# Performance work log

Hardware: AMD Instinct MI355X
Metric: run time of the kernel (lower is better)

Reference implementation:

```python
import jax, jax.numpy as jnp
import numpy as np

BSZ, TSZ, IN_DIM = 32, 1500, 512
G, E = 2, 320            # num_codebooks, num_codebook_entries
OUT_DIM = 768
D = OUT_DIM // G         # entry_dim = 384
TAU = 2.0                # max_temp * decay**0, num_updates starts at 0
EPS = 1e-7
GUMBEL_EPS = 1e-10


def setup_inputs() -> dict:
    key = jax.random.key(0)
    k1, k2, k3, k4 = jax.random.split(key, 4)
    x = jax.random.normal(k1, (BSZ, TSZ, IN_DIM), dtype=jnp.float32)
    W = jax.random.normal(k2, (G * E, IN_DIM), dtype=jnp.float32)  # normal(0,1) init
    b = jnp.zeros((G * E,), dtype=jnp.float32)
    entries = jax.random.uniform(k3, (1, G * E, D), dtype=jnp.float32)
    gumbel_u = jax.random.uniform(k4, (BSZ * TSZ * G, E), dtype=jnp.float32)
    return {"x": x, "W": W, "b": b, "entries": entries, "gumbel_u": gumbel_u}


def reference(x, W, b, entries, gumbel_u):
    bsz, tsz, _ = x.shape
    N = bsz * tsz
    # entry projection -> logits over all codebook entries
    logits = jnp.einsum('btf,ef->bte', x, W) + b            # [B,T,G*E]
    logits = logits.reshape(N * G, E)

    # hard one-hot via argmax (code perplexity stats)
    k = jnp.argmax(logits, axis=-1)                         # [N*G]
    hard_x = jax.nn.one_hot(k, E, dtype=logits.dtype).reshape(N, G, E)
    hard_probs = jnp.mean(hard_x, axis=0)                   # [G,E]
    code_perplexity = jnp.exp(-jnp.sum(hard_probs * jnp.log(hard_probs + EPS), axis=-1)).sum()

    # soft distribution stats (prob perplexity)
    avg_probs = jax.nn.softmax(logits.reshape(N, G, E), axis=-1).mean(axis=0)  # [G,E]
    prob_perplexity = jnp.exp(-jnp.sum(avg_probs * jnp.log(avg_probs + EPS), axis=-1)).sum()

    # gumbel-softmax straight-through (training path)
    g = -jnp.log(-jnp.log(gumbel_u + GUMBEL_EPS) + GUMBEL_EPS)  # gumbel noise from uniforms
    y_soft = jax.nn.softmax((logits + g) / TAU, axis=-1)        # [N*G,E]
    k_g = jnp.argmax(y_soft, axis=-1)
    y_hard = jax.nn.one_hot(k_g, E, dtype=y_soft.dtype)
    y = y_hard + y_soft - jax.lax.stop_gradient(y_soft)        # straight-through

    cb = y.reshape(N, G * E)
    # one-hot-weighted sum over codebook entries
    quantized = jnp.einsum('nge,ged->ngd', y.reshape(N, G, E), entries.reshape(G, E, D))
    quantized = quantized.reshape(bsz, tsz, G * D)             # [B,T,OUT_DIM]
    return quantized, cb, code_perplexity, prob_perplexity
```

## Files before the change

kernel.cpp:

```cpp
#include <hip/hip_runtime.h>
#include <math.h>
#include <stdint.h>

#define NROWS 48000
#define KDIM 512
#define NE 320
#define GE 640
#define DDIM 384
#define ODIM 768
#define CB_OFF 36864000ul
#define SC_OFF 67584000ul
#define MARGIN 4e-3f

using f16x8 = __attribute__((ext_vector_type(8))) _Float16;
using f32x4 = __attribute__((ext_vector_type(4))) float;

#define GLD16(gp, lp)                                                          \
    __builtin_amdgcn_global_load_lds(                                          \
        (const __attribute__((address_space(1))) uint32_t*)(gp),               \
        (__attribute__((address_space(3))) uint32_t*)(lp), 16, 0, 0)

__global__ __launch_bounds__(256) void split16(const float* __restrict__ src,
                                               _Float16* __restrict__ hi,
                                               _Float16* __restrict__ lo,
                                               int n8)
{
    int i = blockIdx.x * 256 + threadIdx.x;
    if (i >= n8) return;
    float4 v0 = *((const float4*)src + 2 * (size_t)i);
    float4 v1 = *((const float4*)src + 2 * (size_t)i + 1);
    float x[8] = {v0.x, v0.y, v0.z, v0.w, v1.x, v1.y, v1.z, v1.w};
    f16x8 h, l;
    #pragma unroll
    for (int k = 0; k < 8; ++k) {
        _Float16 hh = (_Float16)x[k];
        h[k] = hh;
        l[k] = (_Float16)(x[k] - (float)hh);
    }
    *(f16x8*)(hi + (size_t)i * 8) = h;
    *(f16x8*)(lo + (size_t)i * 8) = l;
}

__global__ __launch_bounds__(256) void gemm_cvt(
    const float* __restrict__ X,
    const _Float16* __restrict__ Wh, const _Float16* __restrict__ Wl,
    const float* __restrict__ bvec, float* __restrict__ Lout)
{
    __shared__ _Float16 lds[16384];
    _Float16* Ahs = lds;
    _Float16* Als = lds + 4096;
    _Float16* Bhs = lds + 8192;
    _Float16* Bls = lds + 12288;

    const int bid = blockIdx.x;
    const int q8 = 1875 / 8, r8 = 1875 % 8;
    const int xcd = bid & 7, wi = bid >> 3;
    const int wg = (xcd < r8 ? xcd * (q8 + 1) : r8 * (q8 + 1) + (xcd - r8) * q8) + wi;
    const int bm = wg / 5, bn = wg % 5;

    const int tid = threadIdx.x;
    const int wid = tid >> 6, lane = tid & 63;
    const int fr = lane & 15, fq = lane >> 4;
    const int wm = (wid >> 1) * 64, wn = (wid & 1) * 64;

    const float*     Ag  = X  + (size_t)(bm * 128) * KDIM;
    const _Float16*  Bhg = Wh + (size_t)(bn * 128) * KDIM;
    const _Float16*  Blg = Wl + (size_t)(bn * 128) * KDIM;

    f32x4 acc[4][4];
    #pragma unroll
    for (int i = 0; i < 4; ++i)
        #pragma unroll
        for (int j = 0; j < 4; ++j)
            acc[i][j] = (f32x4){0.f, 0.f, 0.f, 0.f};

    for (int kk = 0; kk < 16; ++kk) {
        const int kh = kk * 32;
        #pragma unroll
        for (int q = 0; q < 2; ++q) {
            const int c = wid * 2 + q;
            const int srow = lane >> 2, sc8 = (lane & 3) * 8;
            const size_t go = (size_t)(c * 16 + srow) * KDIM + kh + sc8;
            GLD16(Bhg + go, Bhs + c * 512);
            GLD16(Blg + go, Bls + c * 512);
        }
        #pragma unroll
        for (int c = 0; c < 2; ++c) {
            const int idx8 = c * 256 + tid;
            const int row = idx8 >> 2, k8 = (idx8 & 3) * 8;
            const float4* xp = (const float4*)(Ag + (size_t)row * KDIM + kh + k8);
            float4 v0 = xp[0], v1 = xp[1];
            float xs[8] = {v0.x, v0.y, v0.z, v0.w, v1.x, v1.y, v1.z, v1.w};
            f16x8 h, l;
            #pragma unroll
            for (int q = 0; q < 8; ++q) {
                _Float16 hh = (_Float16)xs[q];
                h[q] = hh;
                l[q] = (_Float16)(xs[q] - (float)hh);
            }
            *(f16x8*)&Ahs[row * 32 + k8] = h;
            *(f16x8*)&Als[row * 32 + k8] = l;
        }
        __syncthreads();

        f16x8 ah[4], al[4], bh[4], bl[4];
        #pragma unroll
        for (int i = 0; i < 4; ++i) {
            const int ro = (wm + i * 16 + fr) * 32 + fq * 8;
            ah[i] = *(const f16x8*)&Ahs[ro];
            al[i] = *(const f16x8*)&Als[ro];
            const int co = (wn + i * 16 + fr) * 32 + fq * 8;
            bh[i] = *(const f16x8*)&Bhs[co];
            bl[i] = *(const f16x8*)&Bls[co];
        }
        #pragma unroll
        for (int i = 0; i < 4; ++i)
            #pragma unroll
            for (int j = 0; j < 4; ++j) {
                acc[i][j] = __builtin_amdgcn_mfma_f32_16x16x32_f16(ah[i], bh[j], acc[i][j], 0, 0, 0);
                acc[i][j] = __builtin_amdgcn_mfma_f32_16x16x32_f16(ah[i], bl[j], acc[i][j], 0, 0, 0);
                acc[i][j] = __builtin_amdgcn_mfma_f32_16x16x32_f16(al[i], bh[j], acc[i][j], 0, 0, 0);
            }
        __syncthreads();
    }

    #pragma unroll
    for (int i = 0; i < 4; ++i) {
        #pragma unroll
        for (int r = 0; r < 4; ++r) {
            const int m = bm * 128 + wm + i * 16 + fq * 4 + r;
            float* orow = Lout + (size_t)m * GE + bn * 128 + wn;
            #pragma unroll
            for (int j = 0; j < 4; ++j) {
                const int n = bn * 128 + wn + j * 16 + fr;
                orow[j * 16 + fr] = acc[i][j][r] + bvec[n];
            }
        }
    }
}

__device__ __forceinline__ bool better(float a, int ia, float b, int ib) {
    return (a > b) || (a == b && ia < ib);
}

__device__ __forceinline__ void top2_half(const float* v, int il,
                                          float& v1, int& i1, float& v2, int& i2)
{
    v1 = -3.4e38f; i1 = 0x7fffffff;
    v2 = -3.4e38f; i2 = 0x7fffffff;
    #pragma unroll
    for (int i = 0; i < 10; ++i) {
        int e = il + 32 * i;
        float x = v[i];
        if (better(x, e, v1, i1)) { v2 = v1; i2 = i1; v1 = x; i1 = e; }
        else if (better(x, e, v2, i2)) { v2 = x; i2 = e; }
    }
    #pragma unroll
    for (int m = 1; m <= 16; m <<= 1) {
        float ov1 = __shfl_xor(v1, m); int oi1 = __shfl_xor(i1, m);
        float ov2 = __shfl_xor(v2, m); int oi2 = __shfl_xor(i2, m);
        float lv; int li;
        if (better(ov1, oi1, v1, i1)) { lv = v1; li = i1; v1 = ov1; i1 = oi1; }
        else { lv = ov1; li = oi1; }
        if (better(lv, li, v2, i2)) { v2 = lv; i2 = li; }
        if (better(ov2, oi2, v2, i2)) { v2 = ov2; i2 = oi2; }
    }
}

__device__ int resolve2(const float* __restrict__ X, const float* __restrict__ W,
                        const float* __restrict__ bvec, const float* __restrict__ Urow,
                        int n, int h, int c1, int c2, bool gum, int il)
{
    const float* xr = X + (size_t)n * KDIM;
    const float* w1 = W + (size_t)(h * NE + c1) * KDIM;
    const float* w2 = W + (size_t)(h * NE + c2) * KDIM;
    double d1 = 0.0, d2 = 0.0;
    #pragma unroll
    for (int j = 0; j < 16; ++j) {
        int k = il + 32 * j;
        double xv = (double)xr[k];
        d1 += xv * (double)w1[k];
        d2 += xv * (double)w2[k];
    }
    #pragma unroll
    for (int m = 1; m <= 16; m <<= 1) {
        d1 += __shfl_xor(d1, m);
        d2 += __shfl_xor(d2, m);
    }
    d1 += (double)bvec[h * NE + c1];
    d2 += (double)bvec[h * NE + c2];
    if (gum) {
        d1 += -log(-log((double)Urow[c1] + 1e-10) + 1e-10);
        d2 += -log(-log((double)Urow[c2] + 1e-10) + 1e-10);
    }
    return (d2 > d1 || (d2 == d1 && c2 < c1)) ? c2 : c1;
}

__global__ __launch_bounds__(256) void epilogue_kernel(
    const float* __restrict__ X, const float* __restrict__ W,
    const float* __restrict__ bvec, const float* __restrict__ entries,
    const float* __restrict__ gumbel, float* __restrict__ out,
    float* __restrict__ gavgp, unsigned int* __restrict__ gcnt)
{
    __shared__ float s_avgp[GE];
    __shared__ unsigned int s_cnt[GE];
    const int tid = threadIdx.x;
    for (int i = tid; i < GE; i += 256) { s_avgp[i] = 0.f; s_cnt[i] = 0u; }
    __syncthreads();

    const int wave = tid >> 6, lane = tid & 63;
    const int h = lane >> 5, il = lane & 31;

    float accp[10];
    #pragma unroll
    for (int i = 0; i < 10; ++i) accp[i] = 0.f;

    float* cb = out + CB_OFF;

    for (int rr = 0; rr < 8; ++rr) {
        const int n = blockIdx.x * 32 + wave * 8 + rr;
        float* Lrow = cb + (size_t)n * GE + h * NE;
        const float* Urow = gumbel + (size_t)(2 * n + h) * NE;

        float lg[10], zg[10];
        #pragma unroll
        for (int i = 0; i < 10; ++i) {
            int e = il + 32 * i;
            lg[i] = Lrow[e];
            float gn = -logf(-logf(Urow[e] + 1e-10f) + 1e-10f);
            zg[i] = lg[i] + gn;
        }

        float pv1, pv2; int pi1, pi2;
        top2_half(lg, il, pv1, pi1, pv2, pi2);
        float gv1, gv2; int gi1, gi2;
        top2_half(zg, il, gv1, gi1, gv2, gi2);

        int k_plain = pi1;
        if (pv1 - pv2 < MARGIN)
            k_plain = resolve2(X, W, bvec, Urow, n, h, pi1, pi2, false, il);
        int k_g = gi1;
        if (gv1 - gv2 < MARGIN)
            k_g = resolve2(X, W, bvec, Urow, n, h, gi1, gi2, true, il);

        float s = 0.f, ex[10];
        #pragma unroll
        for (int i = 0; i < 10; ++i) { ex[i] = expf(lg[i] - pv1); s += ex[i]; }
        #pragma unroll
        for (int m = 1; m <= 16; m <<= 1) s += __shfl_xor(s, m);
        float inv = 1.f / s;
        #pragma unroll
        for (int i = 0; i < 10; ++i) accp[i] += ex[i] * inv;

        if (il == 0) atomicAdd(&s_cnt[h * NE + k_plain], 1u);

        #pragma unroll
        for (int i = 0; i < 10; ++i) {
            int e = il + 32 * i;
            Lrow[e] = (e == k_g) ? 1.f : 0.f;
        }
        const float* ent = entries + (size_t)(h * NE + k_g) * DDIM;
        float* qrow = out + (size_t)n * ODIM + h * DDIM;
        #pragma unroll
        for (int j = 0; j < 12; ++j) {
            int d = il + 32 * j;
            qrow[d] = ent[d];
        }
    }

    #pragma unroll
    for (int i = 0; i < 10; ++i)
        atomicAdd(&s_avgp[h * NE + il + 32 * i], accp[i]);
    __syncthreads();
    for (int i = tid; i < GE; i += 256) {
        atomicAdd(&gavgp[i], s_avgp[i]);
        unsigned int c = s_cnt[i];
        if (c) atomicAdd(&gcnt[i], c);
    }
}

__global__ void finalize_kernel(const float* __restrict__ gavgp,
                                const unsigned int* __restrict__ gcnt,
                                float* __restrict__ out)
{
    __shared__ double sc[GE], sp[GE];
    const int t = threadIdx.x;
    if (t < GE) {
        double hp = (double)gcnt[t] * (1.0 / 48000.0);
        sc[t] = hp * log(hp + 1e-7);
        double ap = (double)gavgp[t] * (1.0 / 48000.0);
        sp[t] = ap * log(ap + 1e-7);
    }
    __syncthreads();
    if (t == 0) {
        double c0 = 0, c1 = 0, p0 = 0, p1 = 0;
        for (int e = 0; e < NE; ++e) { c0 += sc[e]; p0 += sp[e]; }
        for (int e = NE; e < GE; ++e) { c1 += sc[e]; p1 += sp[e]; }
        out[SC_OFF]     = (float)(exp(-c0) + exp(-c1));
        out[SC_OFF + 1] = (float)(exp(-p0) + exp(-p1));
    }
}

extern "C" void kernel_launch(void* const* d_in, const int* in_sizes, int n_in,
                              void* d_out, int out_size, void* d_ws, size_t ws_size,
                              hipStream_t stream)
{
    const float* X       = (const float*)d_in[0];
    const float* Wf      = (const float*)d_in[1];
    const float* bvec    = (const float*)d_in[2];
    const float* entries = (const float*)d_in[3];
    const float* gumbel  = (const float*)d_in[4];
    float* out = (float*)d_out;

    float* gavgp = (float*)d_ws;
    unsigned int* gcnt = (unsigned int*)((char*)d_ws + 2560);
    _Float16* Wh = (_Float16*)((char*)d_ws + 8192);
    _Float16* Wl = (_Float16*)((char*)d_ws + 8192 + 655360);

    hipMemsetAsync(d_ws, 0, 8192, stream);
    split16<<<160, 256, 0, stream>>>(Wf, Wh, Wl, 40960);
    gemm_cvt<<<1875, 256, 0, stream>>>(X, Wh, Wl, bvec, out + CB_OFF);
    epilogue_kernel<<<1500, 256, 0, stream>>>(X, Wf, bvec, entries, gumbel, out, gavgp, gcnt);
    finalize_kernel<<<1, 640, 0, stream>>>(gavgp, gcnt, out);
}
```

Before: 274.7 us.

## Fuse epilogue into GEMM via per-panel completion counters

```diff
diff --git a/kernel.cpp b/kernel.cpp
--- a/kernel.cpp
+++ b/kernel.cpp
@@ -41,10 +41,70 @@
     *(f16x8*)(lo + (size_t)i * 8) = l;
 }
 
-__global__ __launch_bounds__(256) void gemm_cvt(
-    const float* __restrict__ X,
+__device__ __forceinline__ bool better(float a, int ia, float b, int ib) {
+    return (a > b) || (a == b && ia < ib);
+}
+
+__device__ __forceinline__ void top2_half(const float* v, int il,
+                                          float& v1, int& i1, float& v2, int& i2)
+{
+    v1 = -3.4e38f; i1 = 0x7fffffff;
+    v2 = -3.4e38f; i2 = 0x7fffffff;
+    #pragma unroll
+    for (int i = 0; i < 10; ++i) {
+        int e = il + 32 * i;
+        float x = v[i];
+        if (better(x, e, v1, i1)) { v2 = v1; i2 = i1; v1 = x; i1 = e; }
+        else if (better(x, e, v2, i2)) { v2 = x; i2 = e; }
+    }
+    #pragma unroll
+    for (int m = 1; m <= 16; m <<= 1) {
+        float ov1 = __shfl_xor(v1, m); int oi1 = __shfl_xor(i1, m);
+        float ov2 = __shfl_xor(v2, m); int oi2 = __shfl_xor(i2, m);
+        float lv; int li;
+        if (better(ov1, oi1, v1, i1)) { lv = v1; li = i1; v1 = ov1; i1 = oi1; }
+        else { lv = ov1; li = oi1; }
+        if (better(lv, li, v2, i2)) { v2 = lv; i2 = li; }
+        if (better(ov2, oi2, v2, i2)) { v2 = ov2; i2 = oi2; }
+    }
+}
+
+__device__ int resolve2(const float* __restrict__ X, const float* __restrict__ W,
+                        const float* __restrict__ bvec, const float* __restrict__ Urow,
+                        int n, int h, int c1, int c2, bool gum, int il)
+{
+    const float* xr = X + (size_t)n * KDIM;
+    const float* w1 = W + (size_t)(h * NE + c1) * KDIM;
+    const float* w2 = W + (size_t)(h * NE + c2) * KDIM;
+    double d1 = 0.0, d2 = 0.0;
+    #pragma unroll
+    for (int j = 0; j < 16; ++j) {
+        int k = il + 32 * j;
+        double xv = (double)xr[k];
+        d1 += xv * (double)w1[k];
+        d2 += xv * (double)w2[k];
+    }
+    #pragma unroll
+    for (int m = 1; m <= 16; m <<= 1) {
+        d1 += __shfl_xor(d1, m);
+        d2 += __shfl_xor(d2, m);
+    }
+    d1 += (double)bvec[h * NE + c1];
+    d2 += (double)bvec[h * NE + c2];
+    if (gum) {
+        d1 += -log(-log((double)Urow[c1] + 1e-10) + 1e-10);
+        d2 += -log(-log((double)Urow[c2] + 1e-10) + 1e-10);
+    }
+    return (d2 > d1 || (d2 == d1 && c2 < c1)) ? c2 : c1;
+}
+
+__global__ __launch_bounds__(256) void gemm_fused(
+    const float* __restrict__ X, const float* __restrict__ Wf,
     const _Float16* __restrict__ Wh, const _Float16* __restrict__ Wl,
-    const float* __restrict__ bvec, float* __restrict__ Lout)
+    const float* __restrict__ bvec, const float* __restrict__ entries,
+    const float* __restrict__ gumbel, float* __restrict__ out,
+    float* __restrict__ gavgp, unsigned int* __restrict__ gcnt,
+    unsigned int* __restrict__ panelcnt)
 {
     __shared__ _Float16 lds[16384];
     _Float16* Ahs = lds;
@@ -124,158 +184,106 @@
         __syncthreads();
     }
 
+    float* cb = out + CB_OFF;
     #pragma unroll
     for (int i = 0; i < 4; ++i) {
         #pragma unroll
         for (int r = 0; r < 4; ++r) {
             const int m = bm * 128 + wm + i * 16 + fq * 4 + r;
-            float* orow = Lout + (size_t)m * GE + bn * 128 + wn;
+            float* orow = cb + (size_t)m * GE + bn * 128 + wn;
             #pragma unroll
-            for (int j = 0; j < 4; ++j) {
-                const int n = bn * 128 + wn + j * 16 + fr;
-                orow[j * 16 + fr] = acc[i][j][r] + bvec[n];
+            for (int j = 0; j < 4; ++j)
+                orow[j * 16 + fr] = acc[i][j][r] + bvec[bn * 128 + wn + j * 16 + fr];
+        }
+    }
+
+    __syncthreads();
+    float*    s_avgp = (float*)lds;
+    unsigned* s_cnt  = (unsigned*)((char*)lds + 2560);
+    unsigned* s_own  = (unsigned*)((char*)lds + 5120);
+    for (int i = tid; i < GE; i += 256) { s_avgp[i] = 0.f; s_cnt[i] = 0u; }
+    if (tid < 4) {
+        __threadfence();
+        unsigned old = __hip_atomic_fetch_add(&panelcnt[bm * 4 + tid], 1u,
+                                              __ATOMIC_ACQ_REL,
+                                              __HIP_MEMORY_SCOPE_AGENT);
+        unsigned o = (old == 4u) ? 1u : 0u;
+        if (o) __threadfence();
+        s_own[tid] = o;
+    }
+    __syncthreads();
+
+    const bool anyown = (s_own[0] | s_own[1] | s_own[2] | s_own[3]) != 0u;
+    if (anyown) {
+        const int h2 = lane >> 5, il = lane & 31;
+        float accp[10];
+        #pragma unroll
+        for (int i = 0; i < 10; ++i) accp[i] = 0.f;
+
+        for (int sp = 0; sp < 4; ++sp) {
+            if (!s_own[sp]) continue;
+            for (int rr = 0; rr < 8; ++rr) {
+                const int n = bm * 128 + sp * 32 + wid * 8 + rr;
+                float* Lrow = cb + (size_t)n * GE + h2 * NE;
+                const float* Urow = gumbel + (size_t)(2 * n + h2) * NE;
+
+                float lg[10], zg[10];
+                #pragma unroll
+                for (int i = 0; i < 10; ++i) {
+                    int e = il + 32 * i;
+                    lg[i] = Lrow[e];
+                    float gn = -logf(-logf(Urow[e] + 1e-10f) + 1e-10f);
+                    zg[i] = lg[i] + gn;
+                }
+
+                float pv1, pv2; int pi1, pi2;
+                top2_half(lg, il, pv1, pi1, pv2, pi2);
+                float gv1, gv2; int gi1, gi2;
+                top2_half(zg, il, gv1, gi1, gv2, gi2);
+
+                int k_plain = pi1;
+                if (pv1 - pv2 < MARGIN)
+                    k_plain = resolve2(X, Wf, bvec, Urow, n, h2, pi1, pi2, false, il);
+                int k_g = gi1;
+                if (gv1 - gv2 < MARGIN)
+                    k_g = resolve2(X, Wf, bvec, Urow, n, h2, gi1, gi2, true, il);
+
+                float s = 0.f, ex[10];
+                #pragma unroll
+                for (int i = 0; i < 10; ++i) { ex[i] = expf(lg[i] - pv1); s += ex[i]; }
+                #pragma unroll
+                for (int m = 1; m <= 16; m <<= 1) s += __shfl_xor(s, m);
+                float inv = 1.f / s;
+                #pragma unroll
+                for (int i = 0; i < 10; ++i) accp[i] += ex[i] * inv;
+
+                if (il == 0) atomicAdd(&s_cnt[h2 * NE + k_plain], 1u);
+
+                #pragma unroll
+                for (int i = 0; i < 10; ++i) {
+                    int e = il + 32 * i;
+                    Lrow[e] = (e == k_g) ? 1.f : 0.f;
+                }
+                const float* ent = entries + (size_t)(h2 * NE + k_g) * DDIM;
+                float* qrow = out + (size_t)n * ODIM + h2 * DDIM;
+                #pragma unroll
+                for (int j = 0; j < 12; ++j) {
+                    int d = il + 32 * j;
+                    qrow[d] = ent[d];
+                }
             }
         }
-    }
-}
-
-__device__ __forceinline__ bool better(float a, int ia, float b, int ib) {
-    return (a > b) || (a == b && ia < ib);
-}
-
-__device__ __forceinline__ void top2_half(const float* v, int il,
-                                          float& v1, int& i1, float& v2, int& i2)
-{
-    v1 = -3.4e38f; i1 = 0x7fffffff;
-    v2 = -3.4e38f; i2 = 0x7fffffff;
-    #pragma unroll
-    for (int i = 0; i < 10; ++i) {
-        int e = il + 32 * i;
-        float x = v[i];
-        if (better(x, e, v1, i1)) { v2 = v1; i2 = i1; v1 = x; i1 = e; }
-        else if (better(x, e, v2, i2)) { v2 = x; i2 = e; }
-    }
-    #pragma unroll
-    for (int m = 1; m <= 16; m <<= 1) {
-        float ov1 = __shfl_xor(v1, m); int oi1 = __shfl_xor(i1, m);
-        float ov2 = __shfl_xor(v2, m); int oi2 = __shfl_xor(i2, m);
-        float lv; int li;
-        if (better(ov1, oi1, v1, i1)) { lv = v1; li = i1; v1 = ov1; i1 = oi1; }
-        else { lv = ov1; li = oi1; }
-        if (better(lv, li, v2, i2)) { v2 = lv; i2 = li; }
-        if (better(ov2, oi2, v2, i2)) { v2 = ov2; i2 = oi2; }
-    }
-}
-
-__device__ int resolve2(const float* __restrict__ X, const float* __restrict__ W,
-                        const float* __restrict__ bvec, const float* __restrict__ Urow,
-                        int n, int h, int c1, int c2, bool gum, int il)
-{
-    const float* xr = X + (size_t)n * KDIM;
-    const float* w1 = W + (size_t)(h * NE + c1) * KDIM;
-    const float* w2 = W + (size_t)(h * NE + c2) * KDIM;
-    double d1 = 0.0, d2 = 0.0;
-    #pragma unroll
-    for (int j = 0; j < 16; ++j) {
-        int k = il + 32 * j;
-        double xv = (double)xr[k];
-        d1 += xv * (double)w1[k];
-        d2 += xv * (double)w2[k];
-    }
-    #pragma unroll
-    for (int m = 1; m <= 16; m <<= 1) {
-        d1 += __shfl_xor(d1, m);
-        d2 += __shfl_xor(d2, m);
-    }
-    d1 += (double)bvec[h * NE + c1];
-    d2 += (double)bvec[h * NE + c2];
-    if (gum) {
-        d1 += -log(-log((double)Urow[c1] + 1e-10) + 1e-10);
-        d2 += -log(-log((double)Urow[c2] + 1e-10) + 1e-10);
-    }
-    return (d2 > d1 || (d2 == d1 && c2 < c1)) ? c2 : c1;
-}
-
-__global__ __launch_bounds__(256) void epilogue_kernel(
-    const float* __restrict__ X, const float* __restrict__ W,
-    const float* __restrict__ bvec, const float* __restrict__ entries,
-    const float* __restrict__ gumbel, float* __restrict__ out,
-    float* __restrict__ gavgp, unsigned int* __restrict__ gcnt)
-{
-    __shared__ float s_avgp[GE];
-    __shared__ unsigned int s_cnt[GE];
-    const int tid = threadIdx.x;
-    for (int i = tid; i < GE; i += 256) { s_avgp[i] = 0.f; s_cnt[i] = 0u; }
-    __syncthreads();
-
-    const int wave = tid >> 6, lane = tid & 63;
-    const int h = lane >> 5, il = lane & 31;
-
-    float accp[10];
-    #pragma unroll
-    for (int i = 0; i < 10; ++i) accp[i] = 0.f;
-
-    float* cb = out + CB_OFF;
-
-    for (int rr = 0; rr < 8; ++rr) {
-        const int n = blockIdx.x * 32 + wave * 8 + rr;
-        float* Lrow = cb + (size_t)n * GE + h * NE;
-        const float* Urow = gumbel + (size_t)(2 * n + h) * NE;
-
-        float lg[10], zg[10];
-        #pragma unroll
-        for (int i = 0; i < 10; ++i) {
-            int e = il + 32 * i;
-            lg[i] = Lrow[e];
-            float gn = -logf(-logf(Urow[e] + 1e-10f) + 1e-10f);
-            zg[i] = lg[i] + gn;
-        }
-
-        float pv1, pv2; int pi1, pi2;
-        top2_half(lg, il, pv1, pi1, pv2, pi2);
-        float gv1, gv2; int gi1, gi2;
-        top2_half(zg, il, gv1, gi1, gv2, gi2);
-
-        int k_plain = pi1;
-        if (pv1 - pv2 < MARGIN)
-            k_plain = resolve2(X, W, bvec, Urow, n, h, pi1, pi2, false, il);
-        int k_g = gi1;
-        if (gv1 - gv2 < MARGIN)
-            k_g = resolve2(X, W, bvec, Urow, n, h, gi1, gi2, true, il);
-
-        float s = 0.f, ex[10];
-        #pragma unroll
-        for (int i = 0; i < 10; ++i) { ex[i] = expf(lg[i] - pv1); s += ex[i]; }
-        #pragma unroll
-        for (int m = 1; m <= 16; m <<= 1) s += __shfl_xor(s, m);
-        float inv = 1.f / s;
-        #pragma unroll
-        for (int i = 0; i < 10; ++i) accp[i] += ex[i] * inv;
-
-        if (il == 0) atomicAdd(&s_cnt[h * NE + k_plain], 1u);
-
-        #pragma unroll
-        for (int i = 0; i < 10; ++i) {
-            int e = il + 32 * i;
-            Lrow[e] = (e == k_g) ? 1.f : 0.f;
-        }
-        const float* ent = entries + (size_t)(h * NE + k_g) * DDIM;
-        float* qrow = out + (size_t)n * ODIM + h * DDIM;
-        #pragma unroll
-        for (int j = 0; j < 12; ++j) {
-            int d = il + 32 * j;
-            qrow[d] = ent[d];
-        }
-    }
-
-    #pragma unroll
-    for (int i = 0; i < 10; ++i)
-        atomicAdd(&s_avgp[h * NE + il + 32 * i], accp[i]);
-    __syncthreads();
-    for (int i = tid; i < GE; i += 256) {
-        atomicAdd(&gavgp[i], s_avgp[i]);
-        unsigned int c = s_cnt[i];
-        if (c) atomicAdd(&gcnt[i], c);
+
+        #pragma unroll
+        for (int i = 0; i < 10; ++i)
+            atomicAdd(&s_avgp[h2 * NE + il + 32 * i], accp[i]);
+        __syncthreads();
+        for (int i = tid; i < GE; i += 256) {
+            float a = s_avgp[i];
+            if (a != 0.f) atomicAdd(&gavgp[i], a);
+            unsigned c = s_cnt[i];
+            if (c) atomicAdd(&gcnt[i], c);
+        }
     }
 }
 
@@ -314,12 +322,13 @@
 
     float* gavgp = (float*)d_ws;
     unsigned int* gcnt = (unsigned int*)((char*)d_ws + 2560);
-    _Float16* Wh = (_Float16*)((char*)d_ws + 8192);
-    _Float16* Wl = (_Float16*)((char*)d_ws + 8192 + 655360);
-
-    hipMemsetAsync(d_ws, 0, 8192, stream);
+    unsigned int* panelcnt = (unsigned int*)((char*)d_ws + 5120);
+    _Float16* Wh = (_Float16*)((char*)d_ws + 11264);
+    _Float16* Wl = (_Float16*)((char*)d_ws + 11264 + 655360);
+
+    hipMemsetAsync(d_ws, 0, 11264, stream);
     split16<<<160, 256, 0, stream>>>(Wf, Wh, Wl, 40960);
-    gemm_cvt<<<1875, 256, 0, stream>>>(X, Wh, Wl, bvec, out + CB_OFF);
-    epilogue_kernel<<<1500, 256, 0, stream>>>(X, Wf, bvec, entries, gumbel, out, gavgp, gcnt);
+    gemm_fused<<<1875, 256, 0, stream>>>(X, Wf, Wh, Wl, bvec, entries,
+                                         gumbel, out, gavgp, gcnt, panelcnt);
     finalize_kernel<<<1, 640, 0, stream>>>(gavgp, gcnt, out);
 }
```

After: 690.5 us. 2.51x slower.

## Vectorize epilogue with float4 loads/stores and 16-lane row groups

Applied to the files above, without the earlier changes.

```diff
diff --git a/kernel.cpp b/kernel.cpp
--- a/kernel.cpp
+++ b/kernel.cpp
@@ -143,52 +143,51 @@
     return (a > b) || (a == b && ia < ib);
 }
 
-__device__ __forceinline__ void top2_half(const float* v, int il,
-                                          float& v1, int& i1, float& v2, int& i2)
-{
-    v1 = -3.4e38f; i1 = 0x7fffffff;
-    v2 = -3.4e38f; i2 = 0x7fffffff;
-    #pragma unroll
-    for (int i = 0; i < 10; ++i) {
-        int e = il + 32 * i;
-        float x = v[i];
-        if (better(x, e, v1, i1)) { v2 = v1; i2 = i1; v1 = x; i1 = e; }
-        else if (better(x, e, v2, i2)) { v2 = x; i2 = e; }
-    }
-    #pragma unroll
-    for (int m = 1; m <= 16; m <<= 1) {
+__device__ __forceinline__ void t2merge(float& v1, int& i1, float& v2, int& i2,
+                                        float ov1, int oi1, float ov2, int oi2)
+{
+    if (better(ov1, oi1, v1, i1)) {
+        float tv = v1; int ti = i1;
+        v1 = ov1; i1 = oi1;
+        if (better(ov2, oi2, tv, ti)) { v2 = ov2; i2 = oi2; }
+        else                          { v2 = tv;  i2 = ti;  }
+    } else if (better(ov1, oi1, v2, i2)) {
+        v2 = ov1; i2 = oi1;
+    }
+}
+
+__device__ __forceinline__ void bfly16(float& v1, int& i1, float& v2, int& i2)
+{
+    #pragma unroll
+    for (int m = 1; m <= 8; m <<= 1) {
         float ov1 = __shfl_xor(v1, m); int oi1 = __shfl_xor(i1, m);
         float ov2 = __shfl_xor(v2, m); int oi2 = __shfl_xor(i2, m);
-        float lv; int li;
-        if (better(ov1, oi1, v1, i1)) { lv = v1; li = i1; v1 = ov1; i1 = oi1; }
-        else { lv = ov1; li = oi1; }
-        if (better(lv, li, v2, i2)) { v2 = lv; i2 = li; }
-        if (better(ov2, oi2, v2, i2)) { v2 = ov2; i2 = oi2; }
-    }
-}
-
-__device__ int resolve2(const float* __restrict__ X, const float* __restrict__ W,
-                        const float* __restrict__ bvec, const float* __restrict__ Urow,
-                        int n, int h, int c1, int c2, bool gum, int il)
+        t2merge(v1, i1, v2, i2, ov1, oi1, ov2, oi2);
+    }
+}
+
+__device__ int resolve16(const float* __restrict__ X, const float* __restrict__ W,
+                         const float* __restrict__ bvec, const float* __restrict__ Urow,
+                         int n, int cb, int c1, int c2, bool gum, int l)
 {
     const float* xr = X + (size_t)n * KDIM;
-    const float* w1 = W + (size_t)(h * NE + c1) * KDIM;
-    const float* w2 = W + (size_t)(h * NE + c2) * KDIM;
+    const float* w1 = W + (size_t)(cb * NE + c1) * KDIM;
+    const float* w2 = W + (size_t)(cb * NE + c2) * KDIM;
     double d1 = 0.0, d2 = 0.0;
     #pragma unroll
-    for (int j = 0; j < 16; ++j) {
-        int k = il + 32 * j;
+    for (int j = 0; j < 32; ++j) {
+        int k = l + 16 * j;
         double xv = (double)xr[k];
         d1 += xv * (double)w1[k];
         d2 += xv * (double)w2[k];
     }
     #pragma unroll
-    for (int m = 1; m <= 16; m <<= 1) {
+    for (int m = 1; m <= 8; m <<= 1) {
         d1 += __shfl_xor(d1, m);
         d2 += __shfl_xor(d2, m);
     }
-    d1 += (double)bvec[h * NE + c1];
-    d2 += (double)bvec[h * NE + c2];
+    d1 += (double)bvec[cb * NE + c1];
+    d2 += (double)bvec[cb * NE + c2];
     if (gum) {
         d1 += -log(-log((double)Urow[c1] + 1e-10) + 1e-10);
         d2 += -log(-log((double)Urow[c2] + 1e-10) + 1e-10);
@@ -208,69 +207,82 @@
     for (int i = tid; i < GE; i += 256) { s_avgp[i] = 0.f; s_cnt[i] = 0u; }
     __syncthreads();
 
-    const int wave = tid >> 6, lane = tid & 63;
-    const int h = lane >> 5, il = lane & 31;
-
-    float accp[10];
-    #pragma unroll
-    for (int i = 0; i < 10; ++i) accp[i] = 0.f;
-
-    float* cb = out + CB_OFF;
+    const int wid = tid >> 6, lane = tid & 63;
+    const int qw = lane >> 4, l = lane & 15;
+    const int cb = qw & 1, rsub = qw >> 1;
+
+    float accp[20];
+    #pragma unroll
+    for (int t = 0; t < 20; ++t) accp[t] = 0.f;
 
     for (int rr = 0; rr < 8; ++rr) {
-        const int n = blockIdx.x * 32 + wave * 8 + rr;
-        float* Lrow = cb + (size_t)n * GE + h * NE;
-        const float* Urow = gumbel + (size_t)(2 * n + h) * NE;
-
-        float lg[10], zg[10];
-        #pragma unroll
-        for (int i = 0; i < 10; ++i) {
-            int e = il + 32 * i;
-            lg[i] = Lrow[e];
-            float gn = -logf(-logf(Urow[e] + 1e-10f) + 1e-10f);
-            zg[i] = lg[i] + gn;
-        }
-
-        float pv1, pv2; int pi1, pi2;
-        top2_half(lg, il, pv1, pi1, pv2, pi2);
-        float gv1, gv2; int gi1, gi2;
-        top2_half(zg, il, gv1, gi1, gv2, gi2);
-
-        int k_plain = pi1;
-        if (pv1 - pv2 < MARGIN)
-            k_plain = resolve2(X, W, bvec, Urow, n, h, pi1, pi2, false, il);
+        const int n = blockIdx.x * 64 + wid * 16 + rr * 2 + rsub;
+        float* Lrow = out + CB_OFF + (size_t)n * GE + cb * NE;
+        const float* Urow = gumbel + (size_t)(2 * n + cb) * NE;
+
+        float lg[20];
+        float v1 = -3.4e38f, v2 = -3.4e38f; int i1 = 0x7fffffff, i2 = 0x7fffffff;
+        float g1 = -3.4e38f, g2 = -3.4e38f; int gi1 = 0x7fffffff, gi2 = 0x7fffffff;
+        #pragma unroll
+        for (int q = 0; q < 5; ++q) {
+            float4 lv = *(const float4*)(Lrow + l * 4 + q * 64);
+            float4 uv = *(const float4*)(Urow + l * 4 + q * 64);
+            float lx[4] = {lv.x, lv.y, lv.z, lv.w};
+            float ux[4] = {uv.x, uv.y, uv.z, uv.w};
+            #pragma unroll
+            for (int c = 0; c < 4; ++c) {
+                float x = lx[c];
+                lg[q * 4 + c] = x;
+                int e = l * 4 + q * 64 + c;
+                if (better(x, e, v1, i1)) { v2 = v1; i2 = i1; v1 = x; i1 = e; }
+                else if (better(x, e, v2, i2)) { v2 = x; i2 = e; }
+                float z = x + (-logf(-logf(ux[c] + 1e-10f) + 1e-10f));
+                if (better(z, e, g1, gi1)) { g2 = g1; gi2 = gi1; g1 = z; gi1 = e; }
+                else if (better(z, e, g2, gi2)) { g2 = z; gi2 = e; }
+            }
+        }
+        bfly16(v1, i1, v2, i2);
+        bfly16(g1, gi1, g2, gi2);
+
+        int k_plain = i1;
+        if (v1 - v2 < MARGIN)
+            k_plain = resolve16(X, W, bvec, Urow, n, cb, i1, i2, false, l);
         int k_g = gi1;
-        if (gv1 - gv2 < MARGIN)
-            k_g = resolve2(X, W, bvec, Urow, n, h, gi1, gi2, true, il);
-
-        float s = 0.f, ex[10];
-        #pragma unroll
-        for (int i = 0; i < 10; ++i) { ex[i] = expf(lg[i] - pv1); s += ex[i]; }
-        #pragma unroll
-        for (int m = 1; m <= 16; m <<= 1) s += __shfl_xor(s, m);
+        if (g1 - g2 < MARGIN)
+            k_g = resolve16(X, W, bvec, Urow, n, cb, gi1, gi2, true, l);
+
+        float s = 0.f, ex[20];
+        #pragma unroll
+        for (int t = 0; t < 20; ++t) { ex[t] = expf(lg[t] - v1); s += ex[t]; }
+        #pragma unroll
+        for (int m = 1; m <= 8; m <<= 1) s += __shfl_xor(s, m);
         float inv = 1.f / s;
         #pragma unroll
-        for (int i = 0; i < 10; ++i) accp[i] += ex[i] * inv;
-
-        if (il == 0) atomicAdd(&s_cnt[h * NE + k_plain], 1u);
-
-        #pragma unroll
-        for (int i = 0; i < 10; ++i) {
-            int e = il + 32 * i;
-            Lrow[e] = (e == k_g) ? 1.f : 0.f;
-        }
-        const float* ent = entries + (size_t)(h * NE + k_g) * DDIM;
-        float* qrow = out + (size_t)n * ODIM + h * DDIM;
-        #pragma unroll
-        for (int j = 0; j < 12; ++j) {
-            int d = il + 32 * j;
-            qrow[d] = ent[d];
-        }
-    }
-
-    #pragma unroll
-    for (int i = 0; i < 10; ++i)
-        atomicAdd(&s_avgp[h * NE + il + 32 * i], accp[i]);
+        for (int t = 0; t < 20; ++t) accp[t] += ex[t] * inv;
+
+        if (l == 0) atomicAdd(&s_cnt[cb * NE + k_plain], 1u);
+
+        #pragma unroll
+        for (int q = 0; q < 5; ++q) {
+            const int c0 = l * 4 + q * 64;
+            float4 v;
+            v.x = (c0     == k_g) ? 1.f : 0.f;
+            v.y = (c0 + 1 == k_g) ? 1.f : 0.f;
+            v.z = (c0 + 2 == k_g) ? 1.f : 0.f;
+            v.w = (c0 + 3 == k_g) ? 1.f : 0.f;
+            *(float4*)(Lrow + c0) = v;
+        }
+        const float4* ent = (const float4*)(entries + (size_t)(cb * NE + k_g) * DDIM);
+        float4* qrow = (float4*)(out + (size_t)n * ODIM + cb * DDIM);
+        #pragma unroll
+        for (int t = 0; t < 6; ++t) qrow[l + t * 16] = ent[l + t * 16];
+    }
+
+    #pragma unroll
+    for (int q = 0; q < 5; ++q)
+        #pragma unroll
+        for (int c = 0; c < 4; ++c)
+            atomicAdd(&s_avgp[cb * NE + l * 4 + q * 64 + c], accp[q * 4 + c]);
     __syncthreads();
     for (int i = tid; i < GE; i += 256) {
         atomicAdd(&gavgp[i], s_avgp[i]);
@@ -320,6 +332,6 @@
     hipMemsetAsync(d_ws, 0, 8192, stream);
     split16<<<160, 256, 0, stream>>>(Wf, Wh, Wl, 40960);
     gemm_cvt<<<1875, 256, 0, stream>>>(X, Wh, Wl, bvec, out + CB_OFF);
-    epilogue_kernel<<<1500, 256, 0, stream>>>(X, Wf, bvec, entries, gumbel, out, gavgp, gcnt);
+    epilogue_kernel<<<750, 256, 0, stream>>>(X, Wf, bvec, entries, gumbel, out, gavgp, gcnt);
     finalize_kernel<<<1, 640, 0, stream>>>(gavgp, gcnt, out);
 }
```

Result: slower. 316.1 us (+15.0%).

## Drop low-part of X in split-fp16 GEMM, widen fp64 top-3 argmax fallback

Applied to the files above, without the earlier changes.

```diff
diff --git a/kernel.cpp b/kernel.cpp
--- a/kernel.cpp
+++ b/kernel.cpp
@@ -10,7 +10,7 @@
 #define ODIM 768
 #define CB_OFF 36864000ul
 #define SC_OFF 67584000ul
-#define MARGIN 4e-3f
+#define MARGIN 0.04f
 
 using f16x8 = __attribute__((ext_vector_type(8))) _Float16;
 using f32x4 = __attribute__((ext_vector_type(4))) float;
@@ -46,11 +46,10 @@
     const _Float16* __restrict__ Wh, const _Float16* __restrict__ Wl,
     const float* __restrict__ bvec, float* __restrict__ Lout)
 {
-    __shared__ _Float16 lds[16384];
+    __shared__ _Float16 lds[12288];
     _Float16* Ahs = lds;
-    _Float16* Als = lds + 4096;
-    _Float16* Bhs = lds + 8192;
-    _Float16* Bls = lds + 12288;
+    _Float16* Bhs = lds + 4096;
+    _Float16* Bls = lds + 8192;
 
     const int bid = blockIdx.x;
     const int q8 = 1875 / 8, r8 = 1875 % 8;
@@ -91,24 +90,18 @@
             const float4* xp = (const float4*)(Ag + (size_t)row * KDIM + kh + k8);
             float4 v0 = xp[0], v1 = xp[1];
             float xs[8] = {v0.x, v0.y, v0.z, v0.w, v1.x, v1.y, v1.z, v1.w};
-            f16x8 h, l;
+            f16x8 h;
             #pragma unroll
-            for (int q = 0; q < 8; ++q) {
-                _Float16 hh = (_Float16)xs[q];
-                h[q] = hh;
-                l[q] = (_Float16)(xs[q] - (float)hh);
-            }
+            for (int q = 0; q < 8; ++q) h[q] = (_Float16)xs[q];
             *(f16x8*)&Ahs[row * 32 + k8] = h;
-            *(f16x8*)&Als[row * 32 + k8] = l;
         }
         __syncthreads();
 
-        f16x8 ah[4], al[4], bh[4], bl[4];
+        f16x8 ah[4], bh[4], bl[4];
         #pragma unroll
         for (int i = 0; i < 4; ++i) {
             const int ro = (wm + i * 16 + fr) * 32 + fq * 8;
             ah[i] = *(const f16x8*)&Ahs[ro];
-            al[i] = *(const f16x8*)&Als[ro];
             const int co = (wn + i * 16 + fr) * 32 + fq * 8;
             bh[i] = *(const f16x8*)&Bhs[co];
             bl[i] = *(const f16x8*)&Bls[co];
@@ -119,7 +112,6 @@
             for (int j = 0; j < 4; ++j) {
                 acc[i][j] = __builtin_amdgcn_mfma_f32_16x16x32_f16(ah[i], bh[j], acc[i][j], 0, 0, 0);
                 acc[i][j] = __builtin_amdgcn_mfma_f32_16x16x32_f16(ah[i], bl[j], acc[i][j], 0, 0, 0);
-                acc[i][j] = __builtin_amdgcn_mfma_f32_16x16x32_f16(al[i], bh[j], acc[i][j], 0, 0, 0);
             }
         __syncthreads();
     }
@@ -143,57 +135,72 @@
     return (a > b) || (a == b && ia < ib);
 }
 
-__device__ __forceinline__ void top2_half(const float* v, int il,
-                                          float& v1, int& i1, float& v2, int& i2)
-{
-    v1 = -3.4e38f; i1 = 0x7fffffff;
-    v2 = -3.4e38f; i2 = 0x7fffffff;
-    #pragma unroll
-    for (int i = 0; i < 10; ++i) {
-        int e = il + 32 * i;
-        float x = v[i];
-        if (better(x, e, v1, i1)) { v2 = v1; i2 = i1; v1 = x; i1 = e; }
-        else if (better(x, e, v2, i2)) { v2 = x; i2 = e; }
-    }
+__device__ __forceinline__ void ins3(float x, int ix,
+                                     float& v1, int& i1, float& v2, int& i2,
+                                     float& v3, int& i3)
+{
+    if (better(x, ix, v1, i1)) { v3 = v2; i3 = i2; v2 = v1; i2 = i1; v1 = x; i1 = ix; }
+    else if (better(x, ix, v2, i2)) { v3 = v2; i3 = i2; v2 = x; i2 = ix; }
+    else if (better(x, ix, v3, i3)) { v3 = x; i3 = ix; }
+}
+
+__device__ __forceinline__ void top3_half(const float* v, int il,
+                                          float& v1, int& i1, float& v2, int& i2,
+                                          float& v3, int& i3)
+{
+    v1 = -3.4e38f; i1 = 0x7ffffffd;
+    v2 = -3.4e38f; i2 = 0x7ffffffe;
+    v3 = -3.4e38f; i3 = 0x7fffffff;
+    #pragma unroll
+    for (int i = 0; i < 10; ++i)
+        ins3(v[i], il + 32 * i, v1, i1, v2, i2, v3, i3);
     #pragma unroll
     for (int m = 1; m <= 16; m <<= 1) {
         float ov1 = __shfl_xor(v1, m); int oi1 = __shfl_xor(i1, m);
         float ov2 = __shfl_xor(v2, m); int oi2 = __shfl_xor(i2, m);
-        float lv; int li;
-        if (better(ov1, oi1, v1, i1)) { lv = v1; li = i1; v1 = ov1; i1 = oi1; }
-        else { lv = ov1; li = oi1; }
-        if (better(lv, li, v2, i2)) { v2 = lv; i2 = li; }
-        if (better(ov2, oi2, v2, i2)) { v2 = ov2; i2 = oi2; }
-    }
-}
-
-__device__ int resolve2(const float* __restrict__ X, const float* __restrict__ W,
+        float ov3 = __shfl_xor(v3, m); int oi3 = __shfl_xor(i3, m);
+        ins3(ov1, oi1, v1, i1, v2, i2, v3, i3);
+        if (better(ov2, oi2, v2, i2)) { v3 = v2; i3 = i2; v2 = ov2; i2 = oi2; }
+        else if (better(ov2, oi2, v3, i3)) { v3 = ov2; i3 = oi2; }
+        if (better(ov3, oi3, v3, i3)) { v3 = ov3; i3 = oi3; }
+    }
+}
+
+__device__ int resolve3(const float* __restrict__ X, const float* __restrict__ W,
                         const float* __restrict__ bvec, const float* __restrict__ Urow,
-                        int n, int h, int c1, int c2, bool gum, int il)
+                        int n, int h, int c1, int c2, int c3, bool gum, int il)
 {
     const float* xr = X + (size_t)n * KDIM;
     const float* w1 = W + (size_t)(h * NE + c1) * KDIM;
     const float* w2 = W + (size_t)(h * NE + c2) * KDIM;
-    double d1 = 0.0, d2 = 0.0;
+    const float* w3 = W + (size_t)(h * NE + c3) * KDIM;
+    double d1 = 0.0, d2 = 0.0, d3 = 0.0;
     #pragma unroll
     for (int j = 0; j < 16; ++j) {
         int k = il + 32 * j;
         double xv = (double)xr[k];
         d1 += xv * (double)w1[k];
         d2 += xv * (double)w2[k];
+        d3 += xv * (double)w3[k];
     }
     #pragma unroll
     for (int m = 1; m <= 16; m <<= 1) {
         d1 += __shfl_xor(d1, m);
         d2 += __shfl_xor(d2, m);
+        d3 += __shfl_xor(d3, m);
     }
     d1 += (double)bvec[h * NE + c1];
     d2 += (double)bvec[h * NE + c2];
+    d3 += (double)bvec[h * NE + c3];
     if (gum) {
         d1 += -log(-log((double)Urow[c1] + 1e-10) + 1e-10);
         d2 += -log(-log((double)Urow[c2] + 1e-10) + 1e-10);
-    }
-    return (d2 > d1 || (d2 == d1 && c2 < c1)) ? c2 : c1;
+        d3 += -log(-log((double)Urow[c3] + 1e-10) + 1e-10);
+    }
+    int kb = c1; double db = d1;
+    if (d2 > db || (d2 == db && c2 < kb)) { kb = c2; db = d2; }
+    if (d3 > db || (d3 == db && c3 < kb)) { kb = c3; db = d3; }
+    return kb;
 }
 
 __global__ __launch_bounds__(256) void epilogue_kernel(
@@ -231,17 +238,17 @@
             zg[i] = lg[i] + gn;
         }
 
-        float pv1, pv2; int pi1, pi2;
-        top2_half(lg, il, pv1, pi1, pv2, pi2);
-        float gv1, gv2; int gi1, gi2;
-        top2_half(zg, il, gv1, gi1, gv2, gi2);
+        float pv1, pv2, pv3; int pi1, pi2, pi3;
+        top3_half(lg, il, pv1, pi1, pv2, pi2, pv3, pi3);
+        float gv1, gv2, gv3; int gi1, gi2, gi3;
+        top3_half(zg, il, gv1, gi1, gv2, gi2, gv3, gi3);
 
         int k_plain = pi1;
         if (pv1 - pv2 < MARGIN)
-            k_plain = resolve2(X, W, bvec, Urow, n, h, pi1, pi2, false, il);
+            k_plain = resolve3(X, W, bvec, Urow, n, h, pi1, pi2, pi3, false, il);
         int k_g = gi1;
         if (gv1 - gv2 < MARGIN)
-            k_g = resolve2(X, W, bvec, Urow, n, h, gi1, gi2, true, il);
+            k_g = resolve3(X, W, bvec, Urow, n, h, gi1, gi2, gi3, true, il);
 
         float s = 0.f, ex[10];
         #pragma unroll
```

After: 768.0 us. 180% more time.
